# Kernel tuning notes

Hardware: AMD Instinct MI355X
Metric: run time of the kernel (lower is better)

## Reference

```python
import jax, jax.numpy as jnp
import numpy as np

RATIO = 2          # BigVGAN Activation1d up/down ratio
K_FILT = 12        # int(6 * ratio // 2) * 2
DILATIONS = (1, 3, 5)


def _kaiser_sinc_filter1d(cutoff, half_width, kernel_size):
    # Faithful port of BigVGAN's kaiser_sinc_filter1d (even kernel path).
    half_size = kernel_size // 2
    delta_f = 4.0 * half_width
    A = 2.285 * (half_size - 1) * np.pi * delta_f + 7.95
    if A > 50.0:
        beta = 0.1102 * (A - 8.7)
    elif A >= 21.0:
        beta = 0.5842 * (A - 21.0) ** 0.4 + 0.07886 * (A - 21.0)
    else:
        beta = 0.0
    window = np.kaiser(kernel_size, beta)              # periodic=False
    time = np.arange(-half_size, half_size) + 0.5       # even kernel size
    filt = 2.0 * cutoff * window * np.sinc(2.0 * cutoff * time)
    filt = filt / filt.sum()
    return jnp.asarray(filt, dtype=jnp.float32)

FILT = _kaiser_sinc_filter1d(0.5 / RATIO, 0.6 / RATIO, K_FILT)


def _depthwise1d(x, filt, stride, lhs_dilation, padding):
    # x: (B, T, C), filt: (k,) shared across channels (depthwise)
    C = x.shape[-1]
    kern = jnp.tile(filt[:, None, None], (1, 1, C))  # (k, 1, C)
    return jax.lax.conv_general_dilated(
        x, kern, window_strides=(stride,), padding=padding,
        lhs_dilation=(lhs_dilation,), feature_group_count=C,
        dimension_numbers=('NLC', 'LIO', 'NLC'))


def upsample2(x):
    # BigVGAN UpSample1d(ratio=2): replicate pad -> conv_transpose -> crop
    pad = K_FILT // RATIO - 1                       # 5
    pad_left = pad * RATIO + (K_FILT - RATIO) // 2  # 15
    pad_right = pad * RATIO + (K_FILT - RATIO + 1) // 2  # 15
    x = jnp.pad(x, ((0, 0), (pad, pad), (0, 0)), mode='edge')
    # conv_transpose(stride=r) == lhs-dilated conv with full padding
    # (filter is symmetric, so no flip needed)
    y = RATIO * _depthwise1d(x, FILT, 1, RATIO, [(K_FILT - 1, K_FILT - 1)])
    return y[:, pad_left:-pad_right, :]  # (B, 2T, C)


def downsample2(x):
    # BigVGAN DownSample1d(ratio=2) == LowPassFilter1d(stride=2)
    pad_left = K_FILT // 2 - 1  # 5 (even kernel)
    pad_right = K_FILT // 2     # 6
    x = jnp.pad(x, ((0, 0), (pad_left, pad_right), (0, 0)), mode='edge')
    return _depthwise1d(x, FILT, RATIO, 1, 'VALID')  # (B, T, C)


def snake(x, log_alpha):
    # alpha_logscale=True: alpha = exp(param); x + (1/alpha) sin^2(alpha x)
    alpha = jnp.exp(log_alpha)  # (C,), broadcasts over (B, T, C)
    return x + (1.0 / (alpha + 1e-9)) * jnp.square(jnp.sin(alpha * x))


def act1d(x, log_alpha):
    return downsample2(snake(upsample2(x), log_alpha))


def wn_conv(x, v, g, b, dilation):
    # weight-norm: kernel = v / ||v||_(0,1) * g, then SAME dilated conv
    norm = jnp.linalg.norm(v, axis=(0, 1))[None, None, :]  # (1,1,Cout)
    kern = (v / norm) * g  # (k, Cin, Cout)
    y = jax.lax.conv_general_dilated(
        x, kern, window_strides=(1,), padding='SAME',
        rhs_dilation=(dilation,), dimension_numbers=('NLC', 'LIO', 'NLC'))
    return y + b


def setup_inputs() -> dict:
    key = jax.random.key(0)
    ks = jax.random.split(key, 7)
    B, T, C, K = 4, 8192, 512, 3
    n = len(DILATIONS)
    x = jax.random.normal(ks[0], (B, T, C), dtype=jnp.float32)
    v1 = jax.random.normal(ks[1], (n, K, C, C), dtype=jnp.float32)
    g1 = jax.random.uniform(ks[2], (n, 1, 1, C), dtype=jnp.float32)
    b1 = 0.01 * jax.random.normal(ks[3], (n, C), dtype=jnp.float32)
    v2 = jax.random.normal(ks[4], (n, K, C, C), dtype=jnp.float32)
    g2 = jax.random.uniform(ks[5], (n, 1, 1, C), dtype=jnp.float32)
    b2 = 0.01 * jax.random.normal(ks[6], (n, C), dtype=jnp.float32)
    alphas = jnp.zeros((2 * n, C), dtype=jnp.float32)  # log-alpha init 0
    return {'x': x, 'v1': v1, 'g1': g1, 'b1': b1,
            'v2': v2, 'g2': g2, 'b2': b2, 'alphas': alphas}


def reference(x, v1, g1, b1, v2, g2, b2, alphas):
    for i, d in enumerate(DILATIONS):
        xt = act1d(x, alphas[2 * i])
        xt = wn_conv(xt, v1[i], g1[i], b1[i], d)
        xt = act1d(xt, alphas[2 * i + 1])
        xt = wn_conv(xt, v2[i], g2[i], b2[i], 1)
        x = xt + x
    return x
```

## Files before the change

kernel.cpp:

```cpp
#include <hip/hip_runtime.h>
#include <math.h>

#define TLEN   8192
#define CCH    512
#define NBATCH 4
#define GUARD_B 8
#define GUARD_T 16
#define XROWS  (TLEN + GUARD_B + GUARD_T)

typedef __attribute__((ext_vector_type(8))) short short8;
typedef __attribute__((ext_vector_type(4))) float f32x4;

struct Filt { float f[12]; };

#define MFMA16(a, b, c) __builtin_amdgcn_mfma_f32_16x16x32_bf16(a, b, c, 0, 0, 0)
#define BARRIER() asm volatile("s_barrier" ::: "memory")
#define VMCNT(n)  asm volatile("s_waitcnt vmcnt(" #n ")" ::: "memory")

__device__ __forceinline__ unsigned short f2bf(float f) {
  unsigned u = __float_as_uint(f);
  unsigned r = (u + 0x7fffu + ((u >> 16) & 1u)) >> 16;
  return (unsigned short)r;
}

__device__ __forceinline__ float bf2f(unsigned short u) {
  return __uint_as_float((unsigned)u << 16);
}

__device__ __forceinline__ float fast_sin(float x) {
  float r = x * 0.15915494309189535f;
  r -= floorf(r);
  return __builtin_amdgcn_sinf(r);
}

__device__ __forceinline__ float snake1(float u, float a, float rcp) {
  float s = fast_sin(a * u);
  return fmaf(rcp * s, s, u);
}

__device__ __forceinline__ void gload16(const void* g, void* l) {
  __builtin_amdgcn_global_load_lds(
      (const __attribute__((address_space(1))) unsigned int*)g,
      (__attribute__((address_space(3))) unsigned int*)l, 16, 0, 0);
}

__global__ __launch_bounds__(256)
void normp_k(const float* __restrict__ v1, const float* __restrict__ v2,
             float* __restrict__ part) {
  __shared__ float red[256];
  const int c  = blockIdx.x;
  const int cc = blockIdx.y;
  const int jc = blockIdx.z;
  const int col = threadIdx.x & 63;
  const int js  = threadIdx.x >> 6;
  const int co = cc * 64 + col;
  const float* v = (c < 3) ? v1 + (size_t)c * 3 * CCH * CCH
                           : v2 + (size_t)(c - 3) * 3 * CCH * CCH;
  const int j0 = jc * 64 + js * 16;
  float s = 0.f;
  #pragma unroll
  for (int jj = 0; jj < 16; ++jj) {
    float w = v[(size_t)(j0 + jj) * CCH + co];
    s = fmaf(w, w, s);
  }
  red[threadIdx.x] = s;
  __syncthreads();
  if (threadIdx.x < 64) {
    float t = red[threadIdx.x] + red[threadIdx.x + 64] +
              red[threadIdx.x + 128] + red[threadIdx.x + 192];
    part[(size_t)(c * CCH + co) * 24 + jc] = t;
  }
}

__global__ __launch_bounds__(256)
void fin_k(const float* __restrict__ part, const float* __restrict__ g1,
           const float* __restrict__ g2, float* __restrict__ scl) {
  const int i = blockIdx.x * 256 + threadIdx.x;
  const int c = i >> 9, co = i & 511;
  float s = 0.f;
  #pragma unroll
  for (int jc = 0; jc < 24; ++jc) s += part[(size_t)i * 24 + jc];
  const float g = (c < 3) ? g1[c * CCH + co] : g2[(c - 3) * CCH + co];
  scl[i] = g / sqrtf(s);
}

__global__ __launch_bounds__(512)
void zguard_k(unsigned short* __restrict__ xb) {
  const int b = blockIdx.x / 24;
  const int g = blockIdx.x % 24;
  const int row = (g < 8) ? g : (TLEN + g);
  xb[((size_t)b * XROWS + row) * CCH + threadIdx.x] = 0;
}

__global__ __launch_bounds__(256)
void wprep_k(const float* __restrict__ v1, const float* __restrict__ v2,
             const float* __restrict__ scl, unsigned short* __restrict__ wp) {
  const int gtid = blockIdx.x * 256 + threadIdx.x;
  const int lane = gtid & 63;
  const int gw = gtid >> 6;
  const int c  = gw / 1536;
  const int r  = gw - c * 1536;
  const int s  = r >> 6;
  const int r2 = r & 63;
  const int coT  = r2 >> 5;
  const int half = (r2 >> 4) & 1;
  const int cb   = r2 & 15;
  const int tap = s % 3, cib = s / 3;
  const int nf = cb >> 1, kk = cb & 1;
  const int co  = coT * 256 + half * 128 + nf * 16 + (lane & 15);
  const int ci0 = cib * 64 + kk * 32 + (lane >> 4) * 8;
  const float* v = (c < 3) ? v1 + (size_t)c * 3 * CCH * CCH
                           : v2 + (size_t)(c - 3) * 3 * CCH * CCH;
  const float sc = scl[c * CCH + co];
  unsigned short o[8];
  #pragma unroll
  for (int j = 0; j < 8; ++j) {
    float w = v[((size_t)tap * CCH + ci0 + j) * CCH + co] * sc;
    o[j] = f2bf(w);
  }
  *reinterpret_cast<short8*>(wp + (size_t)gw * 512 + lane * 8) =
      *reinterpret_cast<const short8*>(o);
}

template<int INBF>
__global__ __launch_bounds__(256)
void act_k(const void* __restrict__ xin, unsigned short* __restrict__ y,
           const float* __restrict__ la, Filt F) {
  const int idx = blockIdx.x * 256 + threadIdx.x;
  const int c  = (idx & 127) << 2;
  const int ts = (idx >> 7) & 2047;
  const int b  = idx >> 18;
  const int t0 = ts * 4;

  auto ldrow = [&](int row) -> f32x4 {
    if constexpr (INBF) {
      const unsigned short* p =
          (const unsigned short*)xin + ((size_t)b * TLEN + row) * CCH + c;
      ushort4 u = *reinterpret_cast<const ushort4*>(p);
      f32x4 r;
      r[0] = bf2f(u.x); r[1] = bf2f(u.y); r[2] = bf2f(u.z); r[3] = bf2f(u.w);
      return r;
    } else {
      const float* p = (const float*)xin + ((size_t)b * TLEN + row) * CCH + c;
      return *reinterpret_cast<const f32x4*>(p);
    }
  };

  float av[4], rv[4];
  #pragma unroll
  for (int ch = 0; ch < 4; ++ch) {
    av[ch] = expf(la[c + ch]);
    rv[ch] = 1.f / (av[ch] + 1e-9f);
  }

  float acc[4][4];

  if (ts >= 2 && ts <= 2045) {
    f32x4 xw[14];
    #pragma unroll
    for (int j = 0; j < 14; ++j) xw[j] = ldrow(t0 - 5 + j);

    #pragma unroll
    for (int ch = 0; ch < 4; ++ch) {
      float s[18];
      #pragma unroll
      for (int mi = 0; mi < 18; ++mi) {
        float u = 0.f;
        if (mi & 1) {
          const int base = (mi - 5) / 2 + 2;
          #pragma unroll
          for (int r = 0; r < 6; ++r) u = fmaf(F.f[2*r], xw[base + r][ch], u);
        } else {
          const int base = (mi - 6) / 2 + 3;
          #pragma unroll
          for (int r = 0; r < 6; ++r) u = fmaf(F.f[2*r+1], xw[base + r][ch], u);
        }
        u *= 2.f;
        s[mi] = snake1(u, av[ch], rv[ch]);
      }
      #pragma unroll
      for (int tt = 0; tt < 4; ++tt) {
        float a = 0.f;
        #pragma unroll
        for (int k = 0; k < 12; ++k) a = fmaf(F.f[k], s[2*tt + k], a);
        acc[tt][ch] = a;
      }
    }
  } else {
    #pragma unroll
    for (int tt = 0; tt < 4; ++tt) {
      const int t = t0 + tt;
      float a0=0.f, a1=0.f, a2=0.f, a3=0.f;
      for (int k = 0; k < 12; ++k) {
        int m  = 2*t + k - 5;
        int mc = m < 0 ? 0 : (m > 2*TLEN - 1 ? 2*TLEN - 1 : m);
        int tp = mc >> 1;
        int odd = mc & 1;
        float u0=0.f,u1=0.f,u2=0.f,u3=0.f;
        #pragma unroll
        for (int r = 0; r < 6; ++r) {
          int i  = odd ? (tp + r - 2) : (tp + r - 3);
          int ic = i < 0 ? 0 : (i > TLEN - 1 ? TLEN - 1 : i);
          float tap = odd ? F.f[2*r+1] : F.f[2*r];
          f32x4 xv = ldrow(ic);
          u0 = fmaf(tap, xv[0], u0); u1 = fmaf(tap, xv[1], u1);
          u2 = fmaf(tap, xv[2], u2); u3 = fmaf(tap, xv[3], u3);
        }
        u0 *= 2.f; u1 *= 2.f; u2 *= 2.f; u3 *= 2.f;
        const float fk = F.f[k];
        a0 = fmaf(fk, snake1(u0,av[0],rv[0]), a0);
        a1 = fmaf(fk, snake1(u1,av[1],rv[1]), a1);
        a2 = fmaf(fk, snake1(u2,av[2],rv[2]), a2);
        a3 = fmaf(fk, snake1(u3,av[3],rv[3]), a3);
      }
      acc[tt][0]=a0; acc[tt][1]=a1; acc[tt][2]=a2; acc[tt][3]=a3;
    }
  }

  #pragma unroll
  for (int tt = 0; tt < 4; ++tt) {
    ushort4 o;
    o.x = f2bf(acc[tt][0]); o.y = f2bf(acc[tt][1]);
    o.z = f2bf(acc[tt][2]); o.w = f2bf(acc[tt][3]);
    *reinterpret_cast<ushort4*>(
        y + ((size_t)b * XROWS + GUARD_B + t0 + tt) * CCH + c) = o;
  }
}

template<int DIL, int MODE>
__global__ __launch_bounds__(512, 2)
void convm_k(const unsigned short* __restrict__ xb,
             const unsigned short* __restrict__ wp,
             const float* __restrict__ bia,
             const float* __restrict__ resf,
             const unsigned short* __restrict__ resb,
             float* __restrict__ outf,
             unsigned short* __restrict__ outb) {
  __shared__ unsigned short Abuf[2][272 * 64];
  __shared__ unsigned short Bbuf[5][16 * 512];

  const int tid  = threadIdx.x;
  const int lane = tid & 63;
  const int wid  = tid >> 6;
  const int wr   = wid >> 2;
  const int wcn  = wid & 3;
  const int hb   = wcn >> 1;

  const int l   = (blockIdx.x & 7) * 32 + (blockIdx.x >> 3);
  const int coT = l & 1;
  const int tb  = l >> 1;
  const int b   = tb >> 5;
  const int t0  = (tb & 31) * 256;
  const int co0 = coT * 256;

  const int qq = lane >> 4;
  const int r0 = lane & 15;

  const int a_r = lane >> 3;
  const int a_c = (lane & 7) ^ a_r;

  const unsigned short* xrow0 =
      xb + ((size_t)b * XROWS + GUARD_B + t0 - 8) * CCH;
  const unsigned short* wpc = wp;

  f32x4 acc[8][4] = {};
  short8 bfr[4][2];

  auto stA = [&](int cib, int i) {
    int G;
    if (i < 4) G = i * 8 + wid;
    else       G = (wid >= 6) ? (26 + wid) : wid;
    const unsigned short* g =
        xrow0 + (size_t)(8 * G + a_r) * CCH + cib * 64 + a_c * 8;
    gload16(g, &Abuf[cib & 1][G * 512]);
  };
  auto stB = [&](int s, int i) {
    const int half = i >> 1, part = i & 1;
    const int pos = (2 * s + half) % 5;
    const unsigned short* g =
        wpc + ((((size_t)s * 2 + coT) * 2 + half) * 16 + part * 8) * 512 + tid * 8;
    gload16(g, &Bbuf[pos][part * 4096 + wid * 512]);
  };
  auto ldB = [&](int s) {
    const int pos = (2 * s + hb) % 5;
    #pragma unroll
    for (int j = 0; j < 4; ++j)
      #pragma unroll
      for (int kk = 0; kk < 2; ++kk) {
        const int chunk = ((wcn & 1) * 4 + j) * 2 + kk;
        bfr[j][kk] = *reinterpret_cast<const short8*>(
            &Bbuf[pos][chunk * 512 + lane * 8]);
      }
  };
  auto ldA = [&](int pa, int tap, int q, short8 (&af)[2][2]) {
    const int tapoff = 8 + (tap - 1) * DIL;
    const int xr = (tapoff + r0) & 7;
    #pragma unroll
    for (int e = 0; e < 2; ++e) {
      const int row = tapoff + wr * 128 + q * 32 + e * 16 + r0;
      #pragma unroll
      for (int kk = 0; kk < 2; ++kk)
        af[e][kk] = *reinterpret_cast<const short8*>(
            &Abuf[pa][row * 64 + ((kk * 4 + qq) ^ xr) * 8]);
    }
  };
  auto mma = [&](int q, short8 (&af)[2][2]) {
    __builtin_amdgcn_s_setprio(1);
    #pragma unroll
    for (int kk = 0; kk < 2; ++kk)
      #pragma unroll
      for (int e = 0; e < 2; ++e)
        #pragma unroll
        for (int j = 0; j < 4; ++j)
          acc[q * 2 + e][j] = MFMA16(af[e][kk], bfr[j][kk], acc[q * 2 + e][j]);
    __builtin_amdgcn_s_setprio(0);
  };

  stA(0, 0); stB(0, 0); stA(0, 1); stB(0, 1);
  stA(0, 2); stB(0, 2); stA(0, 3); stB(0, 3); stA(0, 4);
  stB(1, 0); stB(1, 1); stB(1, 2); stB(1, 3);
  VMCNT(4);
  BARRIER();

  for (int c = 0; c < 8; ++c) {
    const int T = 3 * c;
    const int pa = c & 1;
    short8 af[2][2];
    const bool more = (c < 7);

    ldB(T);
    ldA(pa, 0, 0, af); stB(T + 2, 0);
    BARRIER(); mma(0, af); BARRIER();
    ldA(pa, 0, 1, af); stB(T + 2, 1);
    BARRIER(); mma(1, af); BARRIER();
    ldA(pa, 0, 2, af); stB(T + 2, 2);
    BARRIER(); mma(2, af); BARRIER();
    ldA(pa, 0, 3, af); stB(T + 2, 3);
    VMCNT(4);
    BARRIER(); mma(3, af); BARRIER();

    ldB(T + 1);
    ldA(pa, 1, 0, af); if (more) { stB(T + 3, 0); stA(c + 1, 0); }
    BARRIER(); mma(0, af); BARRIER();
    ldA(pa, 1, 1, af); if (more) { stB(T + 3, 1); stA(c + 1, 1); }
    BARRIER(); mma(1, af); BARRIER();
    ldA(pa, 1, 2, af); if (more) { stB(T + 3, 2); stA(c + 1, 2); }
    BARRIER(); mma(2, af); BARRIER();
    ldA(pa, 1, 3, af); if (more) { stB(T + 3, 3); stA(c + 1, 3); }
    if (more) { VMCNT(8); } else { VMCNT(0); }
    BARRIER(); mma(3, af); BARRIER();

    ldB(T + 2);
    ldA(pa, 2, 0, af); if (more) { stA(c + 1, 4); stB(T + 4, 0); }
    BARRIER(); mma(0, af); BARRIER();
    ldA(pa, 2, 1, af); if (more) stB(T + 4, 1);
    BARRIER(); mma(1, af); BARRIER();
    ldA(pa, 2, 2, af); if (more) stB(T + 4, 2);
    BARRIER(); mma(2, af); BARRIER();
    ldA(pa, 2, 3, af);
    if (more) { stB(T + 4, 3); VMCNT(4); }
    BARRIER(); mma(3, af); BARRIER();
  }

  #pragma unroll
  for (int j = 0; j < 4; ++j) {
    const int co = co0 + wcn * 64 + j * 16 + r0;
    const float bv = bia[co];
    #pragma unroll
    for (int i = 0; i < 8; ++i) {
      const int t = t0 + wr * 128 + i * 16 + qq * 4;
      #pragma unroll
      for (int e = 0; e < 4; ++e) {
        const size_t off = ((size_t)b * TLEN + t + e) * CCH + co;
        float o = acc[i][j][e] + bv;
        if constexpr (MODE == 1) o += resf[off];
        if constexpr (MODE == 2 || MODE == 3) o += bf2f(resb[off]);
        if constexpr (MODE == 3) outf[off] = o;
        else                     outb[off] = f2bf(o);
      }
    }
  }
}

static double bessel_i0(double x) {
  double t = 1.0, s = 1.0, q = x * x * 0.25;
  for (int k = 1; k < 64; ++k) {
    t *= q / ((double)k * (double)k);
    s += t;
    if (t < 1e-18 * s) break;
  }
  return s;
}

static void make_filter(Filt* F) {
  const double cutoff = 0.25, hw = 0.3;
  const int ks = 12, half = 6;
  const double A = 2.285 * (half - 1) * M_PI * (4.0 * hw) + 7.95;
  double beta;
  if (A > 50.0)       beta = 0.1102 * (A - 8.7);
  else if (A >= 21.0) beta = 0.5842 * pow(A - 21.0, 0.4) + 0.07886 * (A - 21.0);
  else                beta = 0.0;
  const double i0b = bessel_i0(beta);
  double f[12], sum = 0.0;
  for (int n = 0; n < 12; ++n) {
    double rr = 2.0 * n / (ks - 1) - 1.0;
    double w  = bessel_i0(beta * sqrt(fmax(0.0, 1.0 - rr * rr))) / i0b;
    double tm = (double)(n - half) + 0.5;
    double sx = 2.0 * cutoff * tm;
    double snc = (sx == 0.0) ? 1.0 : sin(M_PI * sx) / (M_PI * sx);
    f[n] = 2.0 * cutoff * w * snc;
    sum += f[n];
  }
  for (int n = 0; n < 12; ++n) F->f[n] = (float)(f[n] / sum);
}

extern "C" void kernel_launch(void* const* d_in, const int* in_sizes, int n_in,
                              void* d_out, int out_size, void* d_ws, size_t ws_size,
                              hipStream_t stream) {
  (void)in_sizes; (void)n_in; (void)out_size; (void)ws_size;
  const float* x  = (const float*)d_in[0];
  const float* v1 = (const float*)d_in[1];
  const float* g1 = (const float*)d_in[2];
  const float* b1 = (const float*)d_in[3];
  const float* v2 = (const float*)d_in[4];
  const float* g2 = (const float*)d_in[5];
  const float* b2 = (const float*)d_in[6];
  const float* al = (const float*)d_in[7];
  float* out = (float*)d_out;

  const size_t N = (size_t)NBATCH * TLEN * CCH;
  unsigned short* wb1  = (unsigned short*)d_ws;
  unsigned short* xbuf = wb1 + N;
  unsigned short* xres = xbuf + (size_t)NBATCH * XROWS * CCH;
  unsigned short* wp   = xres + N;
  float* part = (float*)(wp + (size_t)6 * 3 * CCH * CCH);
  float* scl  = part + (size_t)6 * CCH * 24;

  Filt F;
  make_filter(&F);

  zguard_k<<<96, 512, 0, stream>>>(xbuf);
  normp_k<<<dim3(6, 8, 24), 256, 0, stream>>>(v1, v2, part);
  fin_k<<<12, 256, 0, stream>>>(part, g1, g2, scl);
  wprep_k<<<2304, 256, 0, stream>>>(v1, v2, scl, wp);

  const int cgrid = NBATCH * (TLEN / 256) * 2;
  const int nblk_act = (NBATCH * 2048 * 128) / 256;
  const size_t wsz = (size_t)3 * CCH * CCH;

  act_k<0><<<nblk_act, 256, 0, stream>>>(x, xbuf, al + 0 * CCH, F);
  convm_k<1, 0><<<cgrid, 512, 0, stream>>>(xbuf, wp + 0 * wsz, b1 + 0 * CCH,
                                           nullptr, nullptr, nullptr, wb1);
  act_k<1><<<nblk_act, 256, 0, stream>>>(wb1, xbuf, al + 1 * CCH, F);
  convm_k<1, 1><<<cgrid, 512, 0, stream>>>(xbuf, wp + 3 * wsz, b2 + 0 * CCH,
                                           x, nullptr, nullptr, xres);

  act_k<1><<<nblk_act, 256, 0, stream>>>(xres, xbuf, al + 2 * CCH, F);
  convm_k<3, 0><<<cgrid, 512, 0, stream>>>(xbuf, wp + 1 * wsz, b1 + 1 * CCH,
                                           nullptr, nullptr, nullptr, wb1);
  act_k<1><<<nblk_act, 256, 0, stream>>>(wb1, xbuf, al + 3 * CCH, F);
  convm_k<1, 2><<<cgrid, 512, 0, stream>>>(xbuf, wp + 4 * wsz, b2 + 1 * CCH,
                                           nullptr, xres, nullptr, xres);

  act_k<1><<<nblk_act, 256, 0, stream>>>(xres, xbuf, al + 4 * CCH, F);
  convm_k<5, 0><<<cgrid, 512, 0, stream>>>(xbuf, wp + 2 * wsz, b1 + 2 * CCH,
                                           nullptr, nullptr, nullptr, wb1);
  act_k<1><<<nblk_act, 256, 0, stream>>>(wb1, xbuf, al + 5 * CCH, F);
  convm_k<1, 3><<<cgrid, 512, 0, stream>>>(xbuf, wp + 5 * wsz, b2 + 2 * CCH,
                                           nullptr, xres, out, nullptr);
}
```

Measured before the change: 648.0 us.

## Restructure conv main loop to cut barriers and double-buffer A fragments

Replaces the per-quarter barrier/mma pattern (eight barriers per tap) with two barriers per tap. It also ping-pongs two A-fragment register sets so LDS reads of the next quarter overlap the MFMAs of the current one. Global-to-LDS staging is reshuffled around the new barriers, with retuned vmcnt waits. This cuts synchronisation stalls and exposed LDS latency, at the cost of more registers and tighter correctness constraints on the buffer reuse timing.

```diff
diff --git a/kernel.cpp b/kernel.cpp
--- a/kernel.cpp
+++ b/kernel.cpp
@@ -304,7 +304,7 @@
             &Abuf[pa][row * 64 + ((kk * 4 + qq) ^ xr) * 8]);
     }
   };
-  auto mma = [&](int q, short8 (&af)[2][2]) {
+  auto mmaQ = [&](int q, short8 (&af)[2][2]) {
     __builtin_amdgcn_s_setprio(1);
     #pragma unroll
     for (int kk = 0; kk < 2; ++kk)
@@ -316,50 +316,44 @@
     __builtin_amdgcn_s_setprio(0);
   };
 
-  stA(0, 0); stB(0, 0); stA(0, 1); stB(0, 1);
-  stA(0, 2); stB(0, 2); stA(0, 3); stB(0, 3); stA(0, 4);
+  stA(0, 0); stA(0, 1); stA(0, 2); stA(0, 3); stA(0, 4);
+  stB(0, 0); stB(0, 1); stB(0, 2); stB(0, 3);
   stB(1, 0); stB(1, 1); stB(1, 2); stB(1, 3);
   VMCNT(4);
   BARRIER();
 
   for (int c = 0; c < 8; ++c) {
-    const int T = 3 * c;
     const int pa = c & 1;
-    short8 af[2][2];
-    const bool more = (c < 7);
-
-    ldB(T);
-    ldA(pa, 0, 0, af); stB(T + 2, 0);
-    BARRIER(); mma(0, af); BARRIER();
-    ldA(pa, 0, 1, af); stB(T + 2, 1);
-    BARRIER(); mma(1, af); BARRIER();
-    ldA(pa, 0, 2, af); stB(T + 2, 2);
-    BARRIER(); mma(2, af); BARRIER();
-    ldA(pa, 0, 3, af); stB(T + 2, 3);
-    VMCNT(4);
-    BARRIER(); mma(3, af); BARRIER();
-
-    ldB(T + 1);
-    ldA(pa, 1, 0, af); if (more) { stB(T + 3, 0); stA(c + 1, 0); }
-    BARRIER(); mma(0, af); BARRIER();
-    ldA(pa, 1, 1, af); if (more) { stB(T + 3, 1); stA(c + 1, 1); }
-    BARRIER(); mma(1, af); BARRIER();
-    ldA(pa, 1, 2, af); if (more) { stB(T + 3, 2); stA(c + 1, 2); }
-    BARRIER(); mma(2, af); BARRIER();
-    ldA(pa, 1, 3, af); if (more) { stB(T + 3, 3); stA(c + 1, 3); }
-    if (more) { VMCNT(8); } else { VMCNT(0); }
-    BARRIER(); mma(3, af); BARRIER();
-
-    ldB(T + 2);
-    ldA(pa, 2, 0, af); if (more) { stA(c + 1, 4); stB(T + 4, 0); }
-    BARRIER(); mma(0, af); BARRIER();
-    ldA(pa, 2, 1, af); if (more) stB(T + 4, 1);
-    BARRIER(); mma(1, af); BARRIER();
-    ldA(pa, 2, 2, af); if (more) stB(T + 4, 2);
-    BARRIER(); mma(2, af); BARRIER();
-    ldA(pa, 2, 3, af);
-    if (more) { stB(T + 4, 3); VMCNT(4); }
-    BARRIER(); mma(3, af); BARRIER();
+    const bool moreA = (c < 7);
+    #pragma unroll
+    for (int tap = 0; tap < 3; ++tap) {
+      const int T = 3 * c + tap;
+      const bool more = (T + 2 < 24);
+
+      ldB(T);
+      if (more) { stB(T + 2, 0); stB(T + 2, 1); }
+      if (moreA) {
+        if (tap == 0)      { stA(c + 1, 0); stA(c + 1, 1); }
+        else if (tap == 1) { stA(c + 1, 2); stA(c + 1, 3); stA(c + 1, 4); }
+      }
+      BARRIER();
+      if (more) { stB(T + 2, 2); stB(T + 2, 3); }
+      {
+        short8 afA[2][2], afB[2][2];
+        ldA(pa, tap, 0, afA);
+        ldA(pa, tap, 1, afB); mmaQ(0, afA);
+        ldA(pa, tap, 2, afA); mmaQ(1, afB);
+        ldA(pa, tap, 3, afB); mmaQ(2, afA);
+        mmaQ(3, afB);
+      }
+      if (T < 21) {
+        if (tap == 0)      { if (moreA) VMCNT(6); else VMCNT(4); }
+        else if (tap == 1) { if (moreA) VMCNT(7); else VMCNT(4); }
+        else               VMCNT(4);
+      } else if (T == 21)  VMCNT(4);
+      else                 VMCNT(0);
+      BARRIER();
+    }
   }
 
   #pragma unroll
```

New measurement: 658.2 us. Within noise of the previous version (+1.6%).
